# Performance work log

Hardware: AMD Instinct MI355X
Metric: run time of the kernel (lower is better)

Reference implementation:

```python
import jax, jax.numpy as jnp
import numpy as np


def setup_inputs() -> dict:
    key = jax.random.key(0)
    k1, k2, k3, k4 = jax.random.split(key, 4)
    B, N, C = 2, 50000, 64
    M, K, H, C_mid = 50000, 16, 8, 16
    input_features = jax.random.normal(k1, (B, N, C), dtype=jnp.float32)
    neighbor_inds = jax.random.randint(k2, (B, M, K), 0, N, dtype=jnp.int64)
    guidance = jax.random.uniform(k3, (B, M, K, H), dtype=jnp.float32)
    weightnet = jax.random.normal(k4, (B, M, K, C_mid), dtype=jnp.float32)
    return {
        "input_features": input_features,
        "neighbor_inds": neighbor_inds,
        "guidance": guidance,
        "weightnet": weightnet,
    }


def reference(input_features, neighbor_inds, guidance, weightnet):
    # input_features: [B, N, C]; neighbor_inds: [B, M, K] (int);
    # guidance: [B, M, K, H]; weightnet: [B, M, K, C_mid]
    B, N, C = input_features.shape
    _, M, K, H = guidance.shape
    C_mid = weightnet.shape[-1]

    # Gather neighbor features per batch: [B, M, K, C]
    gathered = jax.vmap(lambda f, idx: f[idx])(input_features, neighbor_inds)

    # Guidance-weighted scaling: channels split into H head groups
    gathered = gathered.reshape(B, M, K, H, C // H) * guidance[..., None]
    gathered = gathered.reshape(B, M, K, C)

    # Aggregate over K neighbors with weightnet: [B, M, C, C_mid] -> [B, M, C*C_mid]
    out = jnp.einsum("bmkc,bmkw->bmcw", gathered, weightnet)
    return out.reshape(B, M, C * C_mid)
```

## Files before the change

### kernel.cpp

```cpp
#include <hip/hip_runtime.h>

constexpr int BB    = 2;
constexpr int NN    = 50000;
constexpr int CC    = 64;
constexpr int MM    = 50000;
constexpr int KK    = 16;
constexpr int HH    = 8;
constexpr int CMID  = 16;

typedef float f32x4 __attribute__((ext_vector_type(4)));

__global__ __launch_bounds__(256) void pcf_kernel(
    const float* __restrict__ feat,
    const int*   __restrict__ inds,
    const float* __restrict__ guid,
    const float* __restrict__ wnet,
    float*       __restrict__ out)
{
    const int wib  = threadIdx.x >> 6;
    const int wid  = blockIdx.x * (blockDim.x >> 6) + wib;
    const int lane = threadIdx.x & 63;
    if (wid >= BB * MM) return;

    const int b = wid / MM;

    const float*  fbase = feat + (size_t)b * NN * CC;
    const int*    idx   = inds + (size_t)wid * KK;
    const float*  gd    = guid + (size_t)wid * KK * HH;
    const f32x4*  wn4   = (const f32x4*)(wnet + (size_t)wid * KK * CMID);

    __shared__ f32x4 swn[4][KK * 4];
    swn[wib][lane] = __builtin_nontemporal_load(&wn4[lane]);

    const int h = lane >> 3;

    int myidx = idx[lane & (KK - 1)];


    float g[KK];
#pragma unroll
    for (int k = 0; k < KK; ++k)
        g[k] = __builtin_nontemporal_load(&gd[k * HH + h]);

    float f[KK];
#pragma unroll
    for (int k = 0; k < KK; ++k) {
        const int id = __shfl(myidx, k);
        f[k] = fbase[(size_t)id * CC + lane];
    }

#pragma unroll
    for (int k = 0; k < KK; ++k)
        asm volatile("" :: "v"(f[k]), "v"(g[k]));


    float acc[CMID];
#pragma unroll
    for (int i = 0; i < CMID; ++i) acc[i] = 0.f;

#pragma unroll
    for (int k = 0; k < KK; ++k) {
        const float fg = f[k] * g[k];

        const f32x4 w0 = swn[wib][k * 4 + 0];
        const f32x4 w1 = swn[wib][k * 4 + 1];
        const f32x4 w2 = swn[wib][k * 4 + 2];
        const f32x4 w3 = swn[wib][k * 4 + 3];

        acc[0]  += fg * w0.x;  acc[1]  += fg * w0.y;
        acc[2]  += fg * w0.z;  acc[3]  += fg * w0.w;
        acc[4]  += fg * w1.x;  acc[5]  += fg * w1.y;
        acc[6]  += fg * w1.z;  acc[7]  += fg * w1.w;
        acc[8]  += fg * w2.x;  acc[9]  += fg * w2.y;
        acc[10] += fg * w2.z;  acc[11] += fg * w2.w;
        acc[12] += fg * w3.x;  acc[13] += fg * w3.y;
        acc[14] += fg * w3.z;  acc[15] += fg * w3.w;
    }

    f32x4* o = (f32x4*)(out + (size_t)wid * (CC * CMID) + (size_t)lane * CMID);
    f32x4 o0 = {acc[0],  acc[1],  acc[2],  acc[3]};
    f32x4 o1 = {acc[4],  acc[5],  acc[6],  acc[7]};
    f32x4 o2 = {acc[8],  acc[9],  acc[10], acc[11]};
    f32x4 o3 = {acc[12], acc[13], acc[14], acc[15]};
    o[0] = o0;
    o[1] = o1;
    o[2] = o2;
    o[3] = o3;
}

extern "C" void kernel_launch(void* const* d_in, const int* in_sizes, int n_in,
                              void* d_out, int out_size, void* d_ws, size_t ws_size,
                              hipStream_t stream) {
    const float* feat = (const float*)d_in[0];
    const int*   inds = (const int*)d_in[1];
    const float* guid = (const float*)d_in[2];
    const float* wnet = (const float*)d_in[3];
    float*       out  = (float*)d_out;

    const int total_waves = BB * MM;
    const int waves_per_block = 4;
    const int blocks = (total_waves + waves_per_block - 1) / waves_per_block;

    pcf_kernel<<<blocks, 256, 0, stream>>>(feat, inds, guid, wnet, out);
}
```

Before: 591.4 us.

## Use persistent grid-stride waves processing two points per iteration

The one-wave-per-point launch becomes a fixed grid of 2048 blocks. Each wave strides over pairs of output points and handles both points of a pair in one iteration. It issues both points' guidance, weightnet and gathered feature loads together before computing, so more memory requests are in flight per wave and launch and wave-setup overhead is amortized. The cost is higher register pressure from doubled per-wave buffers and doubled LDS. It also reuses the per-wave LDS slot across iterations without any synchronization.

```diff
diff --git a/kernel.cpp b/kernel.cpp
--- a/kernel.cpp
+++ b/kernel.cpp
@@ -7,6 +7,8 @@
 constexpr int KK    = 16;
 constexpr int HH    = 8;
 constexpr int CMID  = 16;
+constexpr int TOTAL = BB * MM;
+constexpr int NPAIRS = TOTAL / 2;
 
 typedef float f32x4 __attribute__((ext_vector_type(4)));
 
@@ -17,75 +19,109 @@
     const float* __restrict__ wnet,
     float*       __restrict__ out)
 {
-    const int wib  = threadIdx.x >> 6;
-    const int wid  = blockIdx.x * (blockDim.x >> 6) + wib;
-    const int lane = threadIdx.x & 63;
-    if (wid >= BB * MM) return;
+    const int wib    = threadIdx.x >> 6;
+    const int lane   = threadIdx.x & 63;
+    const int wslot  = blockIdx.x * 4 + wib;
+    const int nslots = gridDim.x * 4;
+    const int h      = lane >> 3;
 
-    const int b = wid / MM;
+    __shared__ f32x4 swn[4][2][KK * 4];
 
-    const float*  fbase = feat + (size_t)b * NN * CC;
-    const int*    idx   = inds + (size_t)wid * KK;
-    const float*  gd    = guid + (size_t)wid * KK * HH;
-    const f32x4*  wn4   = (const f32x4*)(wnet + (size_t)wid * KK * CMID);
-
-    __shared__ f32x4 swn[4][KK * 4];
-    swn[wib][lane] = __builtin_nontemporal_load(&wn4[lane]);
-
-    const int h = lane >> 3;
-
-    int myidx = idx[lane & (KK - 1)];
+    for (int pr = wslot; pr < NPAIRS; pr += nslots) {
+        const int pA = pr * 2;
+        const int b  = pA / MM;
 
 
-    float g[KK];
+        const int* idxp = inds + (size_t)pA * KK;
+        int myidx = idxp[lane & 31];
+
+        const float* gdA = guid + (size_t)pA * KK * HH;
+        const float* gdB = gdA + KK * HH;
+        float gA[KK], gB[KK];
 #pragma unroll
-    for (int k = 0; k < KK; ++k)
-        g[k] = __builtin_nontemporal_load(&gd[k * HH + h]);
+        for (int k = 0; k < KK; ++k)
+            gA[k] = __builtin_nontemporal_load(&gdA[k * HH + h]);
+#pragma unroll
+        for (int k = 0; k < KK; ++k)
+            gB[k] = __builtin_nontemporal_load(&gdB[k * HH + h]);
 
-    float f[KK];
+        const f32x4* wp = (const f32x4*)(wnet + (size_t)pA * KK * CMID);
+        swn[wib][0][lane] = __builtin_nontemporal_load(&wp[lane]);
+        swn[wib][1][lane] = __builtin_nontemporal_load(&wp[64 + lane]);
+
+        const float* fbase = feat + (size_t)b * NN * CC;
+        float fA[KK], fB[KK];
 #pragma unroll
-    for (int k = 0; k < KK; ++k) {
-        const int id = __shfl(myidx, k);
-        f[k] = fbase[(size_t)id * CC + lane];
-    }
+        for (int k = 0; k < KK; ++k) {
+            const int id = __shfl(myidx, k);
+            fA[k] = fbase[(size_t)id * CC + lane];
+        }
+#pragma unroll
+        for (int k = 0; k < KK; ++k) {
+            const int id = __shfl(myidx, 16 + k);
+            fB[k] = fbase[(size_t)id * CC + lane];
+        }
 
 #pragma unroll
-    for (int k = 0; k < KK; ++k)
-        asm volatile("" :: "v"(f[k]), "v"(g[k]));
+        for (int k = 0; k < KK; ++k)
+            asm volatile("" :: "v"(fA[k]), "v"(fB[k]), "v"(gA[k]), "v"(gB[k]));
 
+        {
+            float acc[CMID];
+#pragma unroll
+            for (int i = 0; i < CMID; ++i) acc[i] = 0.f;
+#pragma unroll
+            for (int k = 0; k < KK; ++k) {
+                const float fg = fA[k] * gA[k];
+                const f32x4 w0 = swn[wib][0][k * 4 + 0];
+                const f32x4 w1 = swn[wib][0][k * 4 + 1];
+                const f32x4 w2 = swn[wib][0][k * 4 + 2];
+                const f32x4 w3 = swn[wib][0][k * 4 + 3];
+                acc[0]  += fg * w0.x;  acc[1]  += fg * w0.y;
+                acc[2]  += fg * w0.z;  acc[3]  += fg * w0.w;
+                acc[4]  += fg * w1.x;  acc[5]  += fg * w1.y;
+                acc[6]  += fg * w1.z;  acc[7]  += fg * w1.w;
+                acc[8]  += fg * w2.x;  acc[9]  += fg * w2.y;
+                acc[10] += fg * w2.z;  acc[11] += fg * w2.w;
+                acc[12] += fg * w3.x;  acc[13] += fg * w3.y;
+                acc[14] += fg * w3.z;  acc[15] += fg * w3.w;
+            }
+            f32x4* o = (f32x4*)(out + (size_t)pA * (CC * CMID) + (size_t)lane * CMID);
+            f32x4 o0 = {acc[0],  acc[1],  acc[2],  acc[3]};
+            f32x4 o1 = {acc[4],  acc[5],  acc[6],  acc[7]};
+            f32x4 o2 = {acc[8],  acc[9],  acc[10], acc[11]};
+            f32x4 o3 = {acc[12], acc[13], acc[14], acc[15]};
+            o[0] = o0; o[1] = o1; o[2] = o2; o[3] = o3;
+        }
 
-    float acc[CMID];
+        {
+            float acc[CMID];
 #pragma unroll
-    for (int i = 0; i < CMID; ++i) acc[i] = 0.f;
-
+            for (int i = 0; i < CMID; ++i) acc[i] = 0.f;
 #pragma unroll
-    for (int k = 0; k < KK; ++k) {
-        const float fg = f[k] * g[k];
-
-        const f32x4 w0 = swn[wib][k * 4 + 0];
-        const f32x4 w1 = swn[wib][k * 4 + 1];
-        const f32x4 w2 = swn[wib][k * 4 + 2];
-        const f32x4 w3 = swn[wib][k * 4 + 3];
-
-        acc[0]  += fg * w0.x;  acc[1]  += fg * w0.y;
-        acc[2]  += fg * w0.z;  acc[3]  += fg * w0.w;
-        acc[4]  += fg * w1.x;  acc[5]  += fg * w1.y;
-        acc[6]  += fg * w1.z;  acc[7]  += fg * w1.w;
-        acc[8]  += fg * w2.x;  acc[9]  += fg * w2.y;
-        acc[10] += fg * w2.z;  acc[11] += fg * w2.w;
-        acc[12] += fg * w3.x;  acc[13] += fg * w3.y;
-        acc[14] += fg * w3.z;  acc[15] += fg * w3.w;
+            for (int k = 0; k < KK; ++k) {
+                const float fg = fB[k] * gB[k];
+                const f32x4 w0 = swn[wib][1][k * 4 + 0];
+                const f32x4 w1 = swn[wib][1][k * 4 + 1];
+                const f32x4 w2 = swn[wib][1][k * 4 + 2];
+                const f32x4 w3 = swn[wib][1][k * 4 + 3];
+                acc[0]  += fg * w0.x;  acc[1]  += fg * w0.y;
+                acc[2]  += fg * w0.z;  acc[3]  += fg * w0.w;
+                acc[4]  += fg * w1.x;  acc[5]  += fg * w1.y;
+                acc[6]  += fg * w1.z;  acc[7]  += fg * w1.w;
+                acc[8]  += fg * w2.x;  acc[9]  += fg * w2.y;
+                acc[10] += fg * w2.z;  acc[11] += fg * w2.w;
+                acc[12] += fg * w3.x;  acc[13] += fg * w3.y;
+                acc[14] += fg * w3.z;  acc[15] += fg * w3.w;
+            }
+            f32x4* o = (f32x4*)(out + (size_t)(pA + 1) * (CC * CMID) + (size_t)lane * CMID);
+            f32x4 o0 = {acc[0],  acc[1],  acc[2],  acc[3]};
+            f32x4 o1 = {acc[4],  acc[5],  acc[6],  acc[7]};
+            f32x4 o2 = {acc[8],  acc[9],  acc[10], acc[11]};
+            f32x4 o3 = {acc[12], acc[13], acc[14], acc[15]};
+            o[0] = o0; o[1] = o1; o[2] = o2; o[3] = o3;
+        }
     }
-
-    f32x4* o = (f32x4*)(out + (size_t)wid * (CC * CMID) + (size_t)lane * CMID);
-    f32x4 o0 = {acc[0],  acc[1],  acc[2],  acc[3]};
-    f32x4 o1 = {acc[4],  acc[5],  acc[6],  acc[7]};
-    f32x4 o2 = {acc[8],  acc[9],  acc[10], acc[11]};
-    f32x4 o3 = {acc[12], acc[13], acc[14], acc[15]};
-    o[0] = o0;
-    o[1] = o1;
-    o[2] = o2;
-    o[3] = o3;
 }
 
 extern "C" void kernel_launch(void* const* d_in, const int* in_sizes, int n_in,
@@ -97,9 +133,6 @@
     const float* wnet = (const float*)d_in[3];
     float*       out  = (float*)d_out;
 
-    const int total_waves = BB * MM;
-    const int waves_per_block = 4;
-    const int blocks = (total_waves + waves_per_block - 1) / waves_per_block;
-
+    const int blocks = 2048;
     pcf_kernel<<<blocks, 256, 0, stream>>>(feat, inds, guid, wnet, out);
 }
```

Result: slower. 611.8 us (+3.5%).
